# Kernel optimization log

Hardware: AMD Instinct MI355X
Metric: run time of the kernel (lower is better)

Reference implementation:

```python
import jax, jax.numpy as jnp
import numpy as np

N = 4096
F_IN = 3
T_DIM = 3
H_DIM = 128
N_HEADS = 4
HEAD_DIM = H_DIM // N_HEADS
OUT_DIM = 128
LN_EPS = 1e-5


def _layernorm(x, g, b):
    mu = jnp.mean(x, axis=-1, keepdims=True)
    var = jnp.mean(jnp.square(x - mu), axis=-1, keepdims=True)
    return (x - mu) * jax.lax.rsqrt(var + LN_EPS) * g + b


def setup_inputs() -> dict:
    key = jax.random.key(0)
    ks = jax.random.split(key, 16)
    enriched = F_IN + T_DIM
    d = {}
    d["node_features"] = jax.random.uniform(ks[0], (N, F_IN), dtype=jnp.float32)
    d["adj_matrix"] = jax.random.uniform(ks[1], (N, N), dtype=jnp.float32)
    d["trigger_context"] = jax.random.uniform(ks[2], (T_DIM,), dtype=jnp.float32)
    # node_projection: Linear(enriched, H_DIM) + LayerNorm
    d["Wp"] = jax.random.normal(ks[3], (H_DIM, enriched), dtype=jnp.float32) * 0.3
    d["bp"] = jnp.zeros((H_DIM,), jnp.float32)
    d["ln1_g"] = jnp.ones((H_DIM,), jnp.float32)
    d["ln1_b"] = jnp.zeros((H_DIM,), jnp.float32)
    # Q/K/V projections (no bias)
    d["Wq"] = jax.random.normal(ks[4], (H_DIM, H_DIM), dtype=jnp.float32) * 0.08
    d["Wk"] = jax.random.normal(ks[5], (H_DIM, H_DIM), dtype=jnp.float32) * 0.08
    d["Wv"] = jax.random.normal(ks[6], (H_DIM, H_DIM), dtype=jnp.float32) * 0.08
    # trigger_temperature: Linear(T_DIM, H_DIM//2) -> ReLU -> Linear(H_DIM//2, N_HEADS) -> Softplus
    d["Wt1"] = jax.random.normal(ks[7], (H_DIM // 2, T_DIM), dtype=jnp.float32) * 0.5
    d["bt1"] = jnp.zeros((H_DIM // 2,), jnp.float32)
    d["Wt2"] = jax.random.normal(ks[8], (N_HEADS, H_DIM // 2), dtype=jnp.float32) * 0.15
    d["bt2"] = jnp.zeros((N_HEADS,), jnp.float32)
    # trigger_gate: Linear(T_DIM, H_DIM) -> Sigmoid
    d["Wg"] = jax.random.normal(ks[9], (H_DIM, T_DIM), dtype=jnp.float32) * 0.5
    d["bg"] = jnp.zeros((H_DIM,), jnp.float32)
    d["stb"] = jnp.zeros((N_HEADS,), jnp.float32)  # stateful_trigger_bias
    # output_projection: Linear(H_DIM, OUT_DIM) + LayerNorm
    d["Wo"] = jax.random.normal(ks[10], (OUT_DIM, H_DIM), dtype=jnp.float32) * 0.08
    d["bo"] = jnp.zeros((OUT_DIM,), jnp.float32)
    d["ln2_g"] = jnp.ones((OUT_DIM,), jnp.float32)
    d["ln2_b"] = jnp.zeros((OUT_DIM,), jnp.float32)
    d["res_scale"] = jnp.ones((1,), jnp.float32) * 0.1
    return d


def reference(node_features, adj_matrix, trigger_context, Wp, bp, ln1_g, ln1_b,
              Wq, Wk, Wv, Wt1, bt1, Wt2, bt2, Wg, bg, stb, Wo, bo,
              ln2_g, ln2_b, res_scale):
    n = node_features.shape[0]
    # 1. Enrichment: concat trigger context to every node
    trig_b = jnp.broadcast_to(trigger_context[None, :], (n, T_DIM))
    enriched = jnp.concatenate([node_features, trig_b], axis=1)  # [N, 6]
    # 2. Projection: Linear -> LayerNorm -> ReLU (dropout identity in eval)
    h = jax.nn.relu(_layernorm(enriched @ Wp.T + bp, ln1_g, ln1_b))  # [N, H_DIM]
    # 3. Multi-head Q/K/V
    Q = (h @ Wq.T).reshape(n, N_HEADS, HEAD_DIM)
    K = (h @ Wk.T).reshape(n, N_HEADS, HEAD_DIM)
    V = (h @ Wv.T).reshape(n, N_HEADS, HEAD_DIM)
    scores = jnp.einsum('ihd,jhd->ijh', Q, K) / jnp.sqrt(jnp.float32(HEAD_DIM))  # [N,N,H]
    # trigger-conditioned temperature per head
    temp = jax.nn.softplus(jax.nn.relu(trigger_context @ Wt1.T + bt1) @ Wt2.T + bt2)
    temp = jnp.clip(temp, 0.1, 5.0)  # [H]
    scores = scores / temp[None, None, :]
    # adjacency mask
    scores = jnp.where((adj_matrix == 0.0)[:, :, None], jnp.float32(-1e9), scores)
    # stateful x trigger interaction bias
    is_reactive = 1.0 - trigger_context[0]
    is_stateful = node_features[:, 2]
    stateful_matrix = jnp.outer(is_stateful, is_stateful)  # [N,N]
    scores = scores + stateful_matrix[:, :, None] * (stb * is_reactive)[None, None, :]
    # softmax over neighbors (dim j)
    attn = jax.nn.softmax(scores, axis=1)  # [N,N,H]
    # trigger gate (scalar mean of sigmoid gate)
    gate_value = jnp.mean(jax.nn.sigmoid(trigger_context @ Wg.T + bg))
    attn = attn * gate_value
    # aggregation
    agg = jnp.einsum('ijh,jhd->ihd', attn, V).reshape(n, H_DIM)
    out = _layernorm(agg @ Wo.T + bo, ln2_g, ln2_b) + res_scale * h[:, :OUT_DIM]
    return out
```

## Files before the change

### kernel.cpp

```cpp
#include <hip/hip_runtime.h>


#define NNODES 4096
#define BI     32
#define JSPLIT 8
#define JCHUNK (NNODES / JSPLIT)
#define NT     (JCHUNK / 32)

typedef float    f32x4 __attribute__((ext_vector_type(4)));
typedef _Float16 f16x8 __attribute__((ext_vector_type(8)));
typedef __fp16   fp16x2 __attribute__((ext_vector_type(2)));

#define P_STF    256
#define P_H      4352
#define P_QH     528640
#define P_KH     790784
#define P_VT     1052928
#define P_PAGG   1315072
#define P_PML    5509376

#define LOG2E 1.4426950408889634f

__device__ __forceinline__ unsigned pk_f16(float lo, float hi) {
  union { fp16x2 h; unsigned u; } c;
  c.h = __builtin_amdgcn_cvt_pkrtz(lo, hi);
  return c.u;
}

__global__ __launch_bounds__(128) void k2_h(
    const float* __restrict__ nf, const float* __restrict__ trig,
    const float* __restrict__ Wp, const float* __restrict__ bp,
    const float* __restrict__ g, const float* __restrict__ b,
    float* __restrict__ ws)
{
  const int i = blockIdx.x, j = threadIdx.x;
  const float t0 = trig[0], t1v = trig[1], t2 = trig[2];
  const float n0 = nf[i*3+0], n1 = nf[i*3+1], n2 = nf[i*3+2];
  const float* wr = Wp + j * 6;
  const float x = bp[j] + n0 * wr[0] + n1 * wr[1] + n2 * wr[2]
                        + t0 * wr[3] + t1v * wr[4] + t2 * wr[5];
  float s = x, sq = x * x;
  for (int off = 1; off < 64; off <<= 1) { s += __shfl_xor(s, off); sq += __shfl_xor(sq, off); }
  __shared__ float red[2][2];
  if ((j & 63) == 0) { red[j >> 6][0] = s; red[j >> 6][1] = sq; }
  __syncthreads();
  const float mu = (red[0][0] + red[1][0]) * (1.f / 128.f);
  const float var = (red[0][1] + red[1][1]) * (1.f / 128.f) - mu * mu;
  const float rs = rsqrtf(var + 1e-5f);
  const float hv = fmaxf((x - mu) * rs * g[j] + b[j], 0.f);
  ws[P_H + (size_t)i * 128 + j] = hv;
  if (j == 0) ws[P_STF + i] = n2;
}

__global__ __launch_bounds__(256) void k3_qkv(
    const float* __restrict__ Wq, const float* __restrict__ Wk,
    const float* __restrict__ Wv, const float* __restrict__ trig,
    const float* __restrict__ Wt1, const float* __restrict__ bt1,
    const float* __restrict__ Wt2, const float* __restrict__ bt2,
    float* __restrict__ ws)
{
  __shared__ float h_s[32][129];
  __shared__ float w_s[32][128];
  __shared__ float o_s[32][132];
  __shared__ float t1_s[64];
  __shared__ float scale_s[4];
  const int t = threadIdx.x;
  const int r0 = blockIdx.x * 32;
  const int mat = blockIdx.y;
  const float* W = (mat == 0) ? Wq : (mat == 1) ? Wk : Wv;
  const float* hp = ws + P_H;

  {
    const int r = t >> 3, kb = (t & 7) << 4;
    const float4* src = (const float4*)(hp + (size_t)(r0 + r) * 128 + kb);
#pragma unroll
    for (int p = 0; p < 4; ++p) {
      float4 v = src[p];
      h_s[r][kb + 4*p + 0] = v.x; h_s[r][kb + 4*p + 1] = v.y;
      h_s[r][kb + 4*p + 2] = v.z; h_s[r][kb + 4*p + 3] = v.w;
    }
  }
  if (t < 64) {
    float a = bt1[t] + trig[0] * Wt1[t*3+0] + trig[1] * Wt1[t*3+1] + trig[2] * Wt1[t*3+2];
    t1_s[t] = fmaxf(a, 0.f);
  }
  __syncthreads();
  if (t < 4) {
    float acc = bt2[t];
    for (int k = 0; k < 64; ++k) acc += Wt2[t*64+k] * t1_s[k];
    float sp = (acc > 20.f) ? acc : log1pf(__expf(acc));
    float temp = fminf(fmaxf(sp, 0.1f), 5.f);
    scale_s[t] = LOG2E / (5.656854249492380f * temp);
  }

  const int rr = t & 31, cs = (t >> 5) << 4;
  float acc[16];
#pragma unroll
  for (int e = 0; e < 16; ++e) acc[e] = 0.f;

  for (int kc = 0; kc < 4; ++kc) {
    __syncthreads();
    {
      const int c = t >> 1, kk = (t & 1) << 4;
      const float4* srcw = (const float4*)(W + c * 128 + kc * 32 + kk);
#pragma unroll
      for (int p = 0; p < 4; ++p) {
        float4 v = srcw[p];
        w_s[kk + 4*p + 0][c] = v.x; w_s[kk + 4*p + 1][c] = v.y;
        w_s[kk + 4*p + 2][c] = v.z; w_s[kk + 4*p + 3][c] = v.w;
      }
    }
    __syncthreads();
#pragma unroll
    for (int k = 0; k < 32; ++k) {
      const float a = h_s[rr][kc * 32 + k];
      const float4 w0 = *(const float4*)&w_s[k][cs + 0];
      const float4 w1 = *(const float4*)&w_s[k][cs + 4];
      const float4 w2 = *(const float4*)&w_s[k][cs + 8];
      const float4 w3 = *(const float4*)&w_s[k][cs + 12];
      acc[0]  += a * w0.x; acc[1]  += a * w0.y; acc[2]  += a * w0.z; acc[3]  += a * w0.w;
      acc[4]  += a * w1.x; acc[5]  += a * w1.y; acc[6]  += a * w1.z; acc[7]  += a * w1.w;
      acc[8]  += a * w2.x; acc[9]  += a * w2.y; acc[10] += a * w2.z; acc[11] += a * w2.w;
      acc[12] += a * w3.x; acc[13] += a * w3.y; acc[14] += a * w3.z; acc[15] += a * w3.w;
    }
  }

  if (mat < 2) {
    unsigned short* dst = (unsigned short*)(ws + (mat == 0 ? P_QH : P_KH));
    const float sc = (mat == 0) ? scale_s[cs >> 5] : 1.f;
    uint4 w0, w1;
    w0.x = pk_f16(acc[0]*sc,  acc[1]*sc);  w0.y = pk_f16(acc[2]*sc,  acc[3]*sc);
    w0.z = pk_f16(acc[4]*sc,  acc[5]*sc);  w0.w = pk_f16(acc[6]*sc,  acc[7]*sc);
    w1.x = pk_f16(acc[8]*sc,  acc[9]*sc);  w1.y = pk_f16(acc[10]*sc, acc[11]*sc);
    w1.z = pk_f16(acc[12]*sc, acc[13]*sc); w1.w = pk_f16(acc[14]*sc, acc[15]*sc);
    *(uint4*)(dst + (size_t)(r0 + rr) * 128 + cs)     = w0;
    *(uint4*)(dst + (size_t)(r0 + rr) * 128 + cs + 8) = w1;
  } else {
#pragma unroll
    for (int e = 0; e < 16; ++e) o_s[rr][cs + e] = acc[e];
    __syncthreads();
    unsigned short* vt = (unsigned short*)(ws + P_VT);
    const int c = t >> 1, rb = (t & 1) << 4;
    float v[16];
#pragma unroll
    for (int mm = 0; mm < 16; ++mm) v[mm] = o_s[rb + mm][c];
    uint4 w0, w1;
    w0.x = pk_f16(v[0],  v[1]);  w0.y = pk_f16(v[2],  v[3]);
    w0.z = pk_f16(v[4],  v[5]);  w0.w = pk_f16(v[6],  v[7]);
    w1.x = pk_f16(v[8],  v[9]);  w1.y = pk_f16(v[10], v[11]);
    w1.z = pk_f16(v[12], v[13]); w1.w = pk_f16(v[14], v[15]);
    *(uint4*)(vt + (size_t)c * 4096 + r0 + rb)     = w0;
    *(uint4*)(vt + (size_t)c * 4096 + r0 + rb + 8) = w1;
  }
}

__global__ __launch_bounds__(256, 4) void k4_attn(
    const float* __restrict__ adj, const float* __restrict__ trig,
    const float* __restrict__ stb, float* __restrict__ ws)
{
  __shared__ float adj_s[2][BI][36];
  const int tid = threadIdx.x;
  const int w = tid >> 6, l = tid & 63, li = l & 15, g = l >> 4;
  const int i0 = blockIdx.x * BI;
  const int jbeg = blockIdx.y * JCHUNK;
  const _Float16* Qh = (const _Float16*)(ws + P_QH);
  const _Float16* Kh = (const _Float16*)(ws + P_KH);
  const _Float16* VT = (const _Float16*)(ws + P_VT);
  const float* stf = ws + P_STF;
  const float stb_eff = stb[w] * (1.f - trig[0]) * LOG2E;

  f16x8 qf[2];
  float a_stb[2], m[2], pls[2];
  f32x4 agg[2][2];
#pragma unroll
  for (int it = 0; it < 2; ++it) {
    qf[it] = *(const f16x8*)(Qh + (size_t)(i0 + it*16 + li) * 128 + w * 32 + g * 8);
    a_stb[it] = stf[i0 + it*16 + li] * stb_eff;
    m[it] = -1e30f; pls[it] = 0.f;
    agg[it][0] = (f32x4){0.f, 0.f, 0.f, 0.f};
    agg[it][1] = (f32x4){0.f, 0.f, 0.f, 0.f};
  }

  const int sr = tid >> 3, sjb = (tid & 7) << 2;
  const float* adj_base = adj + (size_t)(i0 + sr) * 4096 + jbeg + sjb;

  f16x8 kf0A, kf1A, kf0B, kf1B;
  uint2 vaA, vbA, vcA, vdA, vaB, vbB, vcB, vdB;
  f32x4 st0A, st1A, st0B, st1B;

#define LOADF(jtv, S) do { \
    kf0##S = *(const f16x8*)(Kh + (size_t)((jtv) + li) * 128 + w * 32 + g * 8); \
    kf1##S = *(const f16x8*)(Kh + (size_t)((jtv) + 16 + li) * 128 + w * 32 + g * 8); \
    const _Float16* vr_ = VT + (size_t)(w * 32 + li) * 4096 + (jtv) + g * 4; \
    va##S = *(const uint2*)vr_;                 vb##S = *(const uint2*)(vr_ + 16); \
    vc##S = *(const uint2*)(vr_ + 16*4096);     vd##S = *(const uint2*)(vr_ + 16*4096 + 16); \
    st0##S = *(const f32x4*)(stf + (jtv) + g * 4); \
    st1##S = *(const f32x4*)(stf + (jtv) + 16 + g * 4); \
  } while (0)

  auto compute = [&](const f16x8& kf0, const f16x8& kf1,
                     const uint2& va, const uint2& vb, const uint2& vc, const uint2& vd,
                     const f32x4& st0, const f32x4& st1, int buf) {
    union { unsigned u[4]; f16x8 h; } vf0, vf1;
    vf0.u[0] = va.x; vf0.u[1] = va.y; vf0.u[2] = vb.x; vf0.u[3] = vb.y;
    vf1.u[0] = vc.x; vf1.u[1] = vc.y; vf1.u[2] = vd.x; vf1.u[3] = vd.y;
#pragma unroll
    for (int it = 0; it < 2; ++it) {
      const f32x4 zero = {0.f, 0.f, 0.f, 0.f};
      f32x4 c0 = __builtin_amdgcn_mfma_f32_16x16x32_f16(kf0, qf[it], zero, 0, 0, 0);
      f32x4 c1 = __builtin_amdgcn_mfma_f32_16x16x32_f16(kf1, qf[it], zero, 0, 0, 0);
      const f32x4 ad0 = *(const f32x4*)&adj_s[buf][it*16 + li][g * 4];
      const f32x4 ad1 = *(const f32x4*)&adj_s[buf][it*16 + li][16 + g * 4];
      float s0[4], s1[4];
#pragma unroll
      for (int e = 0; e < 4; ++e) {
        s0[e] = ((ad0[e] == 0.f) ? -1e9f : c0[e]) + a_stb[it] * st0[e];
        s1[e] = ((ad1[e] == 0.f) ? -1e9f : c1[e]) + a_stb[it] * st1[e];
      }
      const float pl = fmaxf(fmaxf(fmaxf(s0[0], s0[1]), fmaxf(s0[2], s0[3])),
                             fmaxf(fmaxf(s1[0], s1[1]), fmaxf(s1[2], s1[3])));
      if (!__all(pl <= m[it])) {
        float mx = fmaxf(pl, __shfl_xor(pl, 16));
        mx = fmaxf(mx, __shfl_xor(mx, 32));
        const float mn = fmaxf(m[it], mx);
        const float f = exp2f(m[it] - mn);
        m[it] = mn;
        pls[it] *= f;
#pragma unroll
        for (int e = 0; e < 4; ++e) { agg[it][0][e] *= f; agg[it][1][e] *= f; }
      }
      float p0[4], p1[4];
#pragma unroll
      for (int e = 0; e < 4; ++e) { p0[e] = exp2f(s0[e] - m[it]); p1[e] = exp2f(s1[e] - m[it]); }
      pls[it] += ((p0[0] + p0[1]) + (p0[2] + p0[3])) + ((p1[0] + p1[1]) + (p1[2] + p1[3]));
      union { unsigned u[4]; f16x8 h; } pb;
      pb.u[0] = pk_f16(p0[0], p0[1]);
      pb.u[1] = pk_f16(p0[2], p0[3]);
      pb.u[2] = pk_f16(p1[0], p1[1]);
      pb.u[3] = pk_f16(p1[2], p1[3]);
      agg[it][0] = __builtin_amdgcn_mfma_f32_16x16x32_f16(vf0.h, pb.h, agg[it][0], 0, 0, 0);
      agg[it][1] = __builtin_amdgcn_mfma_f32_16x16x32_f16(vf1.h, pb.h, agg[it][1], 0, 0, 0);
    }
  };

  f32x4 rg = __builtin_nontemporal_load((const f32x4*)adj_base);
  *(f32x4*)&adj_s[0][sr][sjb] = rg;
  LOADF(jbeg, A);

  for (int t = 0; t < NT; t += 2) {
    rg = __builtin_nontemporal_load((const f32x4*)(adj_base + (t + 1) * 32));
    __syncthreads();
    LOADF(jbeg + (t + 1) * 32, B);
    compute(kf0A, kf1A, vaA, vbA, vcA, vdA, st0A, st1A, 0);
    *(f32x4*)&adj_s[1][sr][sjb] = rg;
    if (t + 2 < NT)
      rg = __builtin_nontemporal_load((const f32x4*)(adj_base + (t + 2) * 32));
    __syncthreads();
    if (t + 2 < NT) LOADF(jbeg + (t + 2) * 32, A);
    compute(kf0B, kf1B, vaB, vbB, vcB, vdB, st0B, st1B, 1);
    if (t + 2 < NT) *(f32x4*)&adj_s[0][sr][sjb] = rg;
  }
#undef LOADF

#pragma unroll
  for (int it = 0; it < 2; ++it) {
    float ls = pls[it];
    ls += __shfl_xor(ls, 16);
    ls += __shfl_xor(ls, 32);
    float* pagg = ws + P_PAGG + ((size_t)(blockIdx.y * 4 + w) * 4096 + (i0 + it*16 + li)) * 32;
    *(f32x4*)(pagg + g * 4)      = agg[it][0];
    *(f32x4*)(pagg + 16 + g * 4) = agg[it][1];
    if (g == 0) {
      float* pml = ws + P_PML + ((size_t)(blockIdx.y * 4 + w) * 4096 + (i0 + it*16 + li)) * 2;
      pml[0] = m[it];
      pml[1] = ls;
    }
  }
}

__global__ __launch_bounds__(256) void k5_out(
    const float* __restrict__ Wo, const float* __restrict__ bo,
    const float* __restrict__ g2, const float* __restrict__ b2,
    const float* __restrict__ res_scale,
    const float* __restrict__ trig, const float* __restrict__ Wg,
    const float* __restrict__ bg,
    float* __restrict__ ws, float* __restrict__ out)
{
  __shared__ float wo_s[64][128];
  __shared__ float agg_s[16][132];
  __shared__ float red[16][16][2];
  __shared__ float mu_s[16], rs_s[16];
  __shared__ float gate_red[2];
  const int t = threadIdx.x;
  const int i0 = blockIdx.x * 16;

  if (t < 128) {
    float gx = bg[t] + trig[0] * Wg[t*3+0] + trig[1] * Wg[t*3+1] + trig[2] * Wg[t*3+2];
    float gs = 1.f / (1.f + __expf(-gx));
    for (int off = 1; off < 64; off <<= 1) gs += __shfl_xor(gs, off);
    if ((t & 63) == 0) gate_red[t >> 6] = gs;
  }
  __syncthreads();
  const float gate = (gate_red[0] + gate_red[1]) * (1.f / 128.f);

  {
    const int hd = t & 127, ih = t >> 7;
    const int h = hd >> 5, d = hd & 31;
    for (int ir = 0; ir < 8; ++ir) {
      const int il = ih * 8 + ir;
      const int i = i0 + il;
      float mv[JSPLIT], lv[JSPLIT];
      float mm = -1e30f;
#pragma unroll
      for (int sp = 0; sp < JSPLIT; ++sp) {
        const float* ml = ws + P_PML + ((size_t)(sp * 4 + h) * 4096 + i) * 2;
        mv[sp] = ml[0]; lv[sp] = ml[1];
        mm = fmaxf(mm, mv[sp]);
      }
      float lt = 0.f, av = 0.f;
#pragma unroll
      for (int sp = 0; sp < JSPLIT; ++sp) {
        const float wgt = exp2f(mv[sp] - mm);
        lt += lv[sp] * wgt;
        av += ws[P_PAGG + ((size_t)(sp * 4 + h) * 4096 + i) * 32 + d] * wgt;
      }
      agg_s[il][hd] = av * gate / lt;
    }
  }

  const int r = t & 15, cs = (t >> 4) << 3;
  float acc[8];
#pragma unroll
  for (int e = 0; e < 8; ++e) acc[e] = bo[cs + e];

  for (int kh = 0; kh < 2; ++kh) {
    __syncthreads();
    {
      const int c = t >> 1, kb = (t & 1) << 5;
      const float4* src = (const float4*)(Wo + c * 128 + kh * 64 + kb);
#pragma unroll
      for (int q = 0; q < 8; ++q) {
        float4 v = src[q];
        wo_s[kb + 4*q + 0][c] = v.x; wo_s[kb + 4*q + 1][c] = v.y;
        wo_s[kb + 4*q + 2][c] = v.z; wo_s[kb + 4*q + 3][c] = v.w;
      }
    }
    __syncthreads();
    for (int k = 0; k < 64; ++k) {
      const float a = agg_s[r][kh * 64 + k];
      const float4 w0 = *(const float4*)&wo_s[k][cs];
      const float4 w1 = *(const float4*)&wo_s[k][cs + 4];
      acc[0] += a * w0.x; acc[1] += a * w0.y; acc[2] += a * w0.z; acc[3] += a * w0.w;
      acc[4] += a * w1.x; acc[5] += a * w1.y; acc[6] += a * w1.z; acc[7] += a * w1.w;
    }
  }

  float s = 0.f, sq = 0.f;
#pragma unroll
  for (int e = 0; e < 8; ++e) { s += acc[e]; sq += acc[e] * acc[e]; }
  red[r][t >> 4][0] = s; red[r][t >> 4][1] = sq;
  __syncthreads();
  if (t < 16) {
    float ss = 0.f, qq = 0.f;
    for (int q = 0; q < 16; ++q) { ss += red[t][q][0]; qq += red[t][q][1]; }
    const float mu = ss * (1.f / 128.f);
    const float var = qq * (1.f / 128.f) - mu * mu;
    mu_s[t] = mu; rs_s[t] = rsqrtf(var + 1e-5f);
  }
  __syncthreads();
  const float mu = mu_s[r], rs = rs_s[r];
  const float rsc = res_scale[0];
  const float* hrow = ws + P_H + (size_t)(i0 + r) * 128 + cs;
  const float4 h0 = *(const float4*)(hrow), h1 = *(const float4*)(hrow + 4);
  const float4 ga = *(const float4*)(g2 + cs), gb = *(const float4*)(g2 + cs + 4);
  const float4 ba = *(const float4*)(b2 + cs), bb = *(const float4*)(b2 + cs + 4);
  float4 o0, o1;
  o0.x = (acc[0] - mu) * rs * ga.x + ba.x + rsc * h0.x;
  o0.y = (acc[1] - mu) * rs * ga.y + ba.y + rsc * h0.y;
  o0.z = (acc[2] - mu) * rs * ga.z + ba.z + rsc * h0.z;
  o0.w = (acc[3] - mu) * rs * ga.w + ba.w + rsc * h0.w;
  o1.x = (acc[4] - mu) * rs * gb.x + bb.x + rsc * h1.x;
  o1.y = (acc[5] - mu) * rs * gb.y + bb.y + rsc * h1.y;
  o1.z = (acc[6] - mu) * rs * gb.z + bb.z + rsc * h1.z;
  o1.w = (acc[7] - mu) * rs * gb.w + bb.w + rsc * h1.w;
  *(float4*)(out + (size_t)(i0 + r) * 128 + cs)     = o0;
  *(float4*)(out + (size_t)(i0 + r) * 128 + cs + 4) = o1;
}

extern "C" void kernel_launch(void* const* d_in, const int* in_sizes, int n_in,
                              void* d_out, int out_size, void* d_ws, size_t ws_size,
                              hipStream_t stream) {
  const float* nf   = (const float*)d_in[0];
  const float* adj  = (const float*)d_in[1];
  const float* trig = (const float*)d_in[2];
  const float* Wp   = (const float*)d_in[3];
  const float* bp   = (const float*)d_in[4];
  const float* ln1g = (const float*)d_in[5];
  const float* ln1b = (const float*)d_in[6];
  const float* Wq   = (const float*)d_in[7];
  const float* Wk   = (const float*)d_in[8];
  const float* Wv   = (const float*)d_in[9];
  const float* Wt1  = (const float*)d_in[10];
  const float* bt1  = (const float*)d_in[11];
  const float* Wt2  = (const float*)d_in[12];
  const float* bt2  = (const float*)d_in[13];
  const float* Wg   = (const float*)d_in[14];
  const float* bg   = (const float*)d_in[15];
  const float* stb  = (const float*)d_in[16];
  const float* Wo   = (const float*)d_in[17];
  const float* bo   = (const float*)d_in[18];
  const float* ln2g = (const float*)d_in[19];
  const float* ln2b = (const float*)d_in[20];
  const float* rsc  = (const float*)d_in[21];
  float* ws  = (float*)d_ws;
  float* out = (float*)d_out;

  hipLaunchKernelGGL(k2_h, dim3(NNODES), dim3(128), 0, stream, nf, trig, Wp, bp, ln1g, ln1b, ws);
  hipLaunchKernelGGL(k3_qkv, dim3(128, 3), dim3(256), 0, stream,
                     Wq, Wk, Wv, trig, Wt1, bt1, Wt2, bt2, ws);
  hipLaunchKernelGGL(k4_attn, dim3(NNODES / BI, JSPLIT), dim3(256), 0, stream, adj, trig, stb, ws);
  hipLaunchKernelGGL(k5_out, dim3(256), dim3(256), 0, stream,
                     Wo, bo, ln2g, ln2b, rsc, trig, Wg, bg, ws, out);
}
```

Before: 228.8 us.

## Store K and V in MFMA-fragment-packed layout for coalesced 16-byte loads

The projection kernel now writes K and V in a layout tiled by head, 32-row tile and 16-row pair, ordered the way the attention kernel's MFMA fragments consume them. Each lane can then fetch its K and V operands with one contiguous 16-byte load per fragment, instead of strided row loads for K and four 8-byte loads from transposed V. This is meant to cut memory transactions and address arithmetic in the attention inner loop. In exchange, the V write-out reads transposed values from shared memory in a more complex pattern.

Result: faster. 208.3 us (-8.9%).

```diff
diff --git a/kernel.cpp b/kernel.cpp
--- a/kernel.cpp
+++ b/kernel.cpp
@@ -125,9 +125,10 @@
     }
   }
 
-  if (mat < 2) {
-    unsigned short* dst = (unsigned short*)(ws + (mat == 0 ? P_QH : P_KH));
-    const float sc = (mat == 0) ? scale_s[cs >> 5] : 1.f;
+  const int tile = r0 >> 5;
+  if (mat == 0) {
+    unsigned short* dst = (unsigned short*)(ws + P_QH);
+    const float sc = scale_s[cs >> 5];
     uint4 w0, w1;
     w0.x = pk_f16(acc[0]*sc,  acc[1]*sc);  w0.y = pk_f16(acc[2]*sc,  acc[3]*sc);
     w0.z = pk_f16(acc[4]*sc,  acc[5]*sc);  w0.w = pk_f16(acc[6]*sc,  acc[7]*sc);
@@ -135,22 +136,36 @@
     w1.z = pk_f16(acc[12]*sc, acc[13]*sc); w1.w = pk_f16(acc[14]*sc, acc[15]*sc);
     *(uint4*)(dst + (size_t)(r0 + rr) * 128 + cs)     = w0;
     *(uint4*)(dst + (size_t)(r0 + rr) * 128 + cs + 8) = w1;
+  } else if (mat == 1) {
+    unsigned short* kp = (unsigned short*)(ws + P_KH);
+    const int li = rr & 15, pair = rr >> 4;
+    const int head = cs >> 5, g0 = (cs & 31) >> 3;
+    uint4 w0, w1;
+    w0.x = pk_f16(acc[0],  acc[1]);  w0.y = pk_f16(acc[2],  acc[3]);
+    w0.z = pk_f16(acc[4],  acc[5]);  w0.w = pk_f16(acc[6],  acc[7]);
+    w1.x = pk_f16(acc[8],  acc[9]);  w1.y = pk_f16(acc[10], acc[11]);
+    w1.z = pk_f16(acc[12], acc[13]); w1.w = pk_f16(acc[14], acc[15]);
+    const size_t base = ((size_t)((head * 128 + tile) * 2 + pair)) * 64;
+    *(uint4*)(kp + (base + (g0 * 16 + li)) * 8)       = w0;
+    *(uint4*)(kp + (base + ((g0 + 1) * 16 + li)) * 8) = w1;
   } else {
 #pragma unroll
     for (int e = 0; e < 16; ++e) o_s[rr][cs + e] = acc[e];
     __syncthreads();
-    unsigned short* vt = (unsigned short*)(ws + P_VT);
-    const int c = t >> 1, rb = (t & 1) << 4;
-    float v[16];
-#pragma unroll
-    for (int mm = 0; mm < 16; ++mm) v[mm] = o_s[rb + mm][c];
-    uint4 w0, w1;
-    w0.x = pk_f16(v[0],  v[1]);  w0.y = pk_f16(v[2],  v[3]);
-    w0.z = pk_f16(v[4],  v[5]);  w0.w = pk_f16(v[6],  v[7]);
-    w1.x = pk_f16(v[8],  v[9]);  w1.y = pk_f16(v[10], v[11]);
-    w1.z = pk_f16(v[12], v[13]); w1.w = pk_f16(v[14], v[15]);
-    *(uint4*)(vt + (size_t)c * 4096 + r0 + rb)     = w0;
-    *(uint4*)(vt + (size_t)c * 4096 + r0 + rb + 8) = w1;
+    unsigned short* vp = (unsigned short*)(ws + P_VT);
+#pragma unroll
+    for (int q = 0; q < 2; ++q) {
+      const int f = t + q * 256;
+      const int head = f >> 7, rem = f & 127, pair = rem >> 6, l = rem & 63;
+      const int g = l >> 4, li = l & 15;
+      const int d = head * 32 + pair * 16 + li;
+      uint4 wv;
+      wv.x = pk_f16(o_s[4*g + 0][d],      o_s[4*g + 1][d]);
+      wv.y = pk_f16(o_s[4*g + 2][d],      o_s[4*g + 3][d]);
+      wv.z = pk_f16(o_s[16 + 4*g + 0][d], o_s[16 + 4*g + 1][d]);
+      wv.w = pk_f16(o_s[16 + 4*g + 2][d], o_s[16 + 4*g + 3][d]);
+      *(uint4*)(vp + (((size_t)((head * 128 + tile) * 2 + pair)) * 64 + l) * 8) = wv;
+    }
   }
 }
 
@@ -163,9 +178,10 @@
   const int w = tid >> 6, l = tid & 63, li = l & 15, g = l >> 4;
   const int i0 = blockIdx.x * BI;
   const int jbeg = blockIdx.y * JCHUNK;
+  const int tbeg = jbeg >> 5;
   const _Float16* Qh = (const _Float16*)(ws + P_QH);
-  const _Float16* Kh = (const _Float16*)(ws + P_KH);
-  const _Float16* VT = (const _Float16*)(ws + P_VT);
+  const _Float16* KP = (const _Float16*)(ws + P_KH);
+  const _Float16* VP = (const _Float16*)(ws + P_VT);
   const float* stf = ws + P_STF;
   const float stb_eff = stb[w] * (1.f - trig[0]) * LOG2E;
 
@@ -183,27 +199,24 @@
 
   const int sr = tid >> 3, sjb = (tid & 7) << 2;
   const float* adj_base = adj + (size_t)(i0 + sr) * 4096 + jbeg + sjb;
-
-  f16x8 kf0A, kf1A, kf0B, kf1B;
-  uint2 vaA, vbA, vcA, vdA, vaB, vbB, vcB, vdB;
+  const int l8 = l * 8;
+
+  f16x8 kf0A, kf1A, kf0B, kf1B, vf0A, vf1A, vf0B, vf1B;
   f32x4 st0A, st1A, st0B, st1B;
 
-#define LOADF(jtv, S) do { \
-    kf0##S = *(const f16x8*)(Kh + (size_t)((jtv) + li) * 128 + w * 32 + g * 8); \
-    kf1##S = *(const f16x8*)(Kh + (size_t)((jtv) + 16 + li) * 128 + w * 32 + g * 8); \
-    const _Float16* vr_ = VT + (size_t)(w * 32 + li) * 4096 + (jtv) + g * 4; \
-    va##S = *(const uint2*)vr_;                 vb##S = *(const uint2*)(vr_ + 16); \
-    vc##S = *(const uint2*)(vr_ + 16*4096);     vd##S = *(const uint2*)(vr_ + 16*4096 + 16); \
-    st0##S = *(const f32x4*)(stf + (jtv) + g * 4); \
-    st1##S = *(const f32x4*)(stf + (jtv) + 16 + g * 4); \
+#define LOADF(tg, S) do { \
+    const size_t kb = ((size_t)(w * 128 + (tg))) * 1024 + l8; \
+    kf0##S = *(const f16x8*)(KP + kb); \
+    kf1##S = *(const f16x8*)(KP + kb + 512); \
+    vf0##S = *(const f16x8*)(VP + kb); \
+    vf1##S = *(const f16x8*)(VP + kb + 512); \
+    st0##S = *(const f32x4*)(stf + (tg) * 32 + g * 4); \
+    st1##S = *(const f32x4*)(stf + (tg) * 32 + 16 + g * 4); \
   } while (0)
 
   auto compute = [&](const f16x8& kf0, const f16x8& kf1,
-                     const uint2& va, const uint2& vb, const uint2& vc, const uint2& vd,
+                     const f16x8& vf0, const f16x8& vf1,
                      const f32x4& st0, const f32x4& st1, int buf) {
-    union { unsigned u[4]; f16x8 h; } vf0, vf1;
-    vf0.u[0] = va.x; vf0.u[1] = va.y; vf0.u[2] = vb.x; vf0.u[3] = vb.y;
-    vf1.u[0] = vc.x; vf1.u[1] = vc.y; vf1.u[2] = vd.x; vf1.u[3] = vd.y;
 #pragma unroll
     for (int it = 0; it < 2; ++it) {
       const f32x4 zero = {0.f, 0.f, 0.f, 0.f};
@@ -238,26 +251,26 @@
       pb.u[1] = pk_f16(p0[2], p0[3]);
       pb.u[2] = pk_f16(p1[0], p1[1]);
       pb.u[3] = pk_f16(p1[2], p1[3]);
-      agg[it][0] = __builtin_amdgcn_mfma_f32_16x16x32_f16(vf0.h, pb.h, agg[it][0], 0, 0, 0);
-      agg[it][1] = __builtin_amdgcn_mfma_f32_16x16x32_f16(vf1.h, pb.h, agg[it][1], 0, 0, 0);
+      agg[it][0] = __builtin_amdgcn_mfma_f32_16x16x32_f16(vf0, pb.h, agg[it][0], 0, 0, 0);
+      agg[it][1] = __builtin_amdgcn_mfma_f32_16x16x32_f16(vf1, pb.h, agg[it][1], 0, 0, 0);
     }
   };
 
   f32x4 rg = __builtin_nontemporal_load((const f32x4*)adj_base);
   *(f32x4*)&adj_s[0][sr][sjb] = rg;
-  LOADF(jbeg, A);
+  LOADF(tbeg, A);
 
   for (int t = 0; t < NT; t += 2) {
     rg = __builtin_nontemporal_load((const f32x4*)(adj_base + (t + 1) * 32));
     __syncthreads();
-    LOADF(jbeg + (t + 1) * 32, B);
-    compute(kf0A, kf1A, vaA, vbA, vcA, vdA, st0A, st1A, 0);
+    LOADF(tbeg + t + 1, B);
+    compute(kf0A, kf1A, vf0A, vf1A, st0A, st1A, 0);
     *(f32x4*)&adj_s[1][sr][sjb] = rg;
     if (t + 2 < NT)
       rg = __builtin_nontemporal_load((const f32x4*)(adj_base + (t + 2) * 32));
     __syncthreads();
-    if (t + 2 < NT) LOADF(jbeg + (t + 2) * 32, A);
-    compute(kf0B, kf1B, vaB, vbB, vcB, vdB, st0B, st1B, 1);
+    if (t + 2 < NT) LOADF(tbeg + t + 2, A);
+    compute(kf0B, kf1B, vf0B, vf1B, st0B, st1B, 1);
     if (t + 2 < NT) *(f32x4*)&adj_s[0][sr][sjb] = rg;
   }
 #undef LOADF
```
